# Kernel optimization log

Measured on AMD Instinct MI355X. Metric: run time of the kernel, lower is better.

The kernel has to match this reference:

```python
import jax, jax.numpy as jnp
import numpy as np

B, S, H = 8, 4096, 1024
E, K = 64, 2
CAP_FACTOR = 1.25
TEMP = 1.0
LBW = 0.01


def setup_inputs() -> dict:
    key = jax.random.key(0)
    k1, k2, k3 = jax.random.split(key, 3)
    x = jax.random.normal(k1, (B, S, H), dtype=jnp.float32)
    gate_w = jax.random.normal(k2, (E, H), dtype=jnp.float32) * 0.02
    expert_w = jax.random.normal(k3, (E, H, H), dtype=jnp.float32) * 0.02
    return {"x": x, "gate_w": gate_w, "expert_w": expert_w}


def _moe_forward(x, gate_w, expert_w):
    b, s, h = x.shape
    xf = x.reshape(-1, h)                      # [N, H]
    N = xf.shape[0]
    capacity = int(N * K / E * CAP_FACTOR)

    # --- gating ---
    logits = xf @ gate_w.T                     # [N, E]
    vals, idx = jax.lax.top_k(logits / TEMP, K)  # [N, K]
    probs = jax.nn.softmax(vals, axis=-1)      # [N, K]

    # --- dispatch: first-come-first-served position within each expert ---
    ef = idx.reshape(-1)                       # [N*K], token-major order (matches torch loop)
    onehot = jax.nn.one_hot(ef, E, dtype=jnp.int32)            # [N*K, E]
    pos = jnp.take_along_axis(jnp.cumsum(onehot, axis=0), ef[:, None], axis=1)[:, 0] - 1
    valid = pos < capacity
    slot = jnp.where(valid, ef * capacity + pos, E * capacity)  # out-of-range -> dropped

    # token_map[e, c] = token_idx * K + k  (or -1 if empty)
    token_map = jnp.full((E * capacity,), -1, dtype=jnp.int32)
    token_map = token_map.at[slot].set(jnp.arange(N * K, dtype=jnp.int32), mode="drop")

    tok = jnp.clip(token_map // K, 0, N - 1)
    filled = token_map >= 0
    expert_inputs = jnp.where(filled[:, None], xf[tok], 0.0)    # [E*cap, H]
    expert_inputs = expert_inputs.reshape(E, capacity, h)

    # --- grouped expert GEMM (no bias; zero rows stay zero) ---
    expert_outputs = jnp.einsum("ech,edh->ecd", expert_inputs, expert_w)  # [E, cap, H]

    # --- combine: weighted scatter-add back to tokens ---
    eo_flat = expert_outputs.reshape(E * capacity, h)
    wk = token_map % K
    weight = jnp.where(filled, probs[tok, jnp.clip(wk, 0, K - 1)], 0.0)
    out_idx = jnp.where(filled, tok, N)        # invalid -> dropped
    output = jnp.zeros((N, h), dtype=xf.dtype).at[out_idx].add(
        weight[:, None] * eo_flat, mode="drop")

    # --- aux load-balancing loss ---
    gate_probs = jax.nn.softmax(logits, axis=-1)
    usage = jnp.bincount(ef, length=E).astype(jnp.float32) / (N * K + 1e-9)
    importance = gate_probs.mean(axis=0)
    aux = jnp.sum(usage * importance) * E
    aux = jnp.minimum(aux * LBW, 1.0)

    return output.reshape(b, s, h), aux


def reference(x, gate_w, expert_w):
    return _moe_forward(x, gate_w, expert_w)
```

## Files before the change

kernel.cpp:

```cpp
#include <hip/hip_runtime.h>
#include <hip/hip_bf16.h>

#define NTOK 32768
#define NE 64
#define HD 1024
#define CAP 1280
#define NKF (NTOK*2)
#define NSLOT (NE*CAP)
#define NTILE 128

typedef __attribute__((ext_vector_type(8))) short bf16x8;
typedef __attribute__((ext_vector_type(4))) short bf16x4;
typedef __attribute__((ext_vector_type(4))) float f32x4;
typedef __attribute__((ext_vector_type(4))) unsigned short u16x4;

__device__ __forceinline__ short f2bf(float f) {
  union { __hip_bfloat16 b; short s; } u;
  u.b = __float2bfloat16(f);
  return u.s;
}
__device__ __forceinline__ float bf2f(unsigned short h) {
  return __uint_as_float(((unsigned)h) << 16);
}

__global__ __launch_bounds__(256) void gating_kernel(const float* __restrict__ x,
                                                     const float* __restrict__ gw,
                                                     float* __restrict__ logits,
                                                     __hip_bfloat16* __restrict__ xb) {
  __shared__ float Xs[64][132];
  __shared__ float Gs[64][132];
  const int tid = threadIdx.x;
  const int tok0 = blockIdx.x * 64;
  const int th = tid >> 4;
  const int te = tid & 15;
  float acc[4][4];
#pragma unroll
  for (int i = 0; i < 4; ++i)
#pragma unroll
    for (int j = 0; j < 4; ++j) acc[i][j] = 0.f;

  for (int k0 = 0; k0 < HD; k0 += 128) {
#pragma unroll
    for (int r = 0; r < 8; ++r) {
      int idx = r * 256 + tid;
      int row = idx >> 5;
      int c = (idx & 31) * 4;
      float4 xv4 = *(const float4*)&x[(size_t)(tok0 + row) * HD + k0 + c];
      *(float4*)&Xs[row][c] = xv4;
      bf16x4 o;
      o[0] = f2bf(xv4.x); o[1] = f2bf(xv4.y); o[2] = f2bf(xv4.z); o[3] = f2bf(xv4.w);
      *(bf16x4*)&xb[(size_t)(tok0 + row) * HD + k0 + c] = o;
      *(float4*)&Gs[row][c] = *(const float4*)&gw[(size_t)row * HD + k0 + c];
    }
    __syncthreads();
#pragma unroll 4
    for (int kk = 0; kk < 32; ++kk) {
      float4 xv[4], gv[4];
#pragma unroll
      for (int i = 0; i < 4; ++i) xv[i] = *(float4*)&Xs[th + i * 16][kk * 4];
#pragma unroll
      for (int j = 0; j < 4; ++j) gv[j] = *(float4*)&Gs[te + j * 16][kk * 4];
#pragma unroll
      for (int i = 0; i < 4; ++i)
#pragma unroll
        for (int j = 0; j < 4; ++j) {
          acc[i][j] = fmaf(xv[i].x, gv[j].x, acc[i][j]);
          acc[i][j] = fmaf(xv[i].y, gv[j].y, acc[i][j]);
          acc[i][j] = fmaf(xv[i].z, gv[j].z, acc[i][j]);
          acc[i][j] = fmaf(xv[i].w, gv[j].w, acc[i][j]);
        }
    }
    __syncthreads();
  }
#pragma unroll
  for (int i = 0; i < 4; ++i)
#pragma unroll
    for (int j = 0; j < 4; ++j)
      logits[(size_t)(tok0 + th + i * 16) * NE + te + j * 16] = acc[i][j];
}

__global__ __launch_bounds__(256) void topk_hist_kernel(const float* __restrict__ logits,
                                                        int2* __restrict__ e01,
                                                        float2* __restrict__ p01,
                                                        float* __restrict__ imp_part,
                                                        int* __restrict__ rank_buf,
                                                        int* __restrict__ hist) {
  __shared__ int wh[4][64];
  const int tid = threadIdx.x;
  const int w = tid >> 6, lane = tid & 63;
  const int t = blockIdx.x * 256 + tid;
  float l[64];
  const float4* lp = (const float4*)(logits + (size_t)t * NE);
#pragma unroll
  for (int i = 0; i < 16; ++i) {
    float4 v = lp[i];
    l[4 * i] = v.x; l[4 * i + 1] = v.y; l[4 * i + 2] = v.z; l[4 * i + 3] = v.w;
  }
  float v1 = -1e30f; int i1 = 0;
#pragma unroll
  for (int j = 0; j < 64; ++j) if (l[j] > v1) { v1 = l[j]; i1 = j; }
  float v2 = -1e30f; int i2 = 0;
#pragma unroll
  for (int j = 0; j < 64; ++j) if (j != i1 && l[j] > v2) { v2 = l[j]; i2 = j; }
  float ex = __expf(v2 - v1);
  float inv2 = 1.f / (1.f + ex);
  e01[t] = make_int2(i1, i2);
  p01[t] = make_float2(inv2, ex * inv2);

  float s = 0.f;
#pragma unroll
  for (int j = 0; j < 64; ++j) s += __expf(l[j] - v1);
  float invs = 1.f / s;
  const int wid = t >> 6;
#pragma unroll
  for (int e = 0; e < 64; ++e) {
    float p = __expf(l[e] - v1) * invs;
#pragma unroll
    for (int off = 32; off; off >>= 1) p += __shfl_xor(p, off);
    if (lane == 0) imp_part[(size_t)wid * 64 + e] = p;
  }

  int r0 = 0, r1 = 0, cnt = 0;
#pragma unroll
  for (int j = 0; j < 64; ++j) {
    int a = __shfl(i1, j);
    int b = __shfl(i2, j);
    int ja = (j < lane);
    r0 += ja & (a == i1);
    r0 += ja & (b == i1);
    r1 += ja & (a == i2);
    r1 += ja & (b == i2);
    cnt += (a == lane) + (b == lane);
  }
  wh[w][lane] = cnt;
  __syncthreads();
#pragma unroll
  for (int ww = 0; ww < 4; ++ww)
    if (ww < w) { r0 += wh[ww][i1]; r1 += wh[ww][i2]; }
  rank_buf[2 * t] = r0;
  rank_buf[2 * t + 1] = r1;
  if (tid < 64)
    hist[blockIdx.x * 64 + tid] = wh[0][tid] + wh[1][tid] + wh[2][tid] + wh[3][tid];
}

__global__ __launch_bounds__(64) void scan_kernel(const int* __restrict__ hist,
                                                  int* __restrict__ tile_off,
                                                  int* __restrict__ counts) {
  const int e = threadIdx.x;
  int run = 0;
  for (int t = 0; t < NTILE; ++t) {
    int h = hist[t * 64 + e];
    tile_off[t * 64 + e] = run;
    run += h;
  }
  counts[e] = run;
}

__global__ __launch_bounds__(256) void place_kernel(const int2* __restrict__ e01,
                                                    const int* __restrict__ rank_buf,
                                                    const int* __restrict__ tile_off,
                                                    int* __restrict__ slot_of,
                                                    int* __restrict__ slot_token) {
  const int tid = threadIdx.x;
  const int i = blockIdx.x * 256 + tid;
  int2 ee = e01[i >> 1];
  const int e = (i & 1) ? ee.y : ee.x;
  const int pos = tile_off[(i >> 9) * 64 + e] + rank_buf[i];
  const int slot = (pos < CAP) ? (e * CAP + pos) : -1;
  slot_of[i] = slot;
  if (slot >= 0) slot_token[slot] = i;
}

__global__ __launch_bounds__(256) void convw_kernel(const float* __restrict__ w,
                                                    __hip_bfloat16* __restrict__ wb) {
  size_t i = ((size_t)blockIdx.x * 256 + threadIdx.x) * 8;
  const size_t stride = (size_t)2048 * 256 * 8;
#pragma unroll 2
  for (int it = 0; it < 16; ++it, i += stride) {
    float4 a = *(const float4*)(w + i);
    float4 b = *(const float4*)(w + i + 4);
    bf16x8 o;
    o[0] = f2bf(a.x); o[1] = f2bf(a.y); o[2] = f2bf(a.z); o[3] = f2bf(a.w);
    o[4] = f2bf(b.x); o[5] = f2bf(b.y); o[6] = f2bf(b.z); o[7] = f2bf(b.w);
    *(bf16x8*)(wb + i) = o;
  }
}

#define ASYNC16(g, l) __builtin_amdgcn_global_load_lds( \
    (const __attribute__((address_space(1))) void*)(g), \
    (__attribute__((address_space(3))) void*)(l), 16, 0, 0)

#define STAGE_A(buf, ks, kcol) do {                                             \
    const int _d = ((buf) * 16384 + (ks) * 8192 + wuni) * 2;                    \
    ASYNC16(arow0 + (kcol) + (ks) * 32 + sw8, (char*)lds + _d);                 \
    ASYNC16(arow1 + (kcol) + (ks) * 32 + sw8, (char*)lds + _d + 8192);          \
  } while (0)

#define STAGE_B(buf, ks, kcol) do {                                             \
    const __hip_bfloat16* _g = B + (size_t)srow * HD + (kcol) + (ks) * 32 + sw8; \
    const int _d = (32768 + (buf) * 16384 + (ks) * 8192 + wuni) * 2;            \
    ASYNC16(_g, (char*)lds + _d);                                               \
    ASYNC16(_g + (size_t)128 * HD, (char*)lds + _d + 8192);                     \
  } while (0)

#define LDA(dst, buf, ks, mi) \
  dst = *(const bf16x8*)(lds + (buf) * 16384 + (ks) * 8192 + (wm * 128 + (mi) * 16 + fr) * 32 + rsw)
#define LDB(dst, buf, ks, ni) \
  dst = *(const bf16x8*)(lds + 32768 + (buf) * 16384 + (ks) * 8192 + (wn * 64 + (ni) * 16 + fr) * 32 + rsw)

#define MFMA_HALF(h)                                                            \
  _Pragma("unroll")                                                             \
  for (int mm = 0; mm < 4; ++mm)                                                \
    _Pragma("unroll")                                                           \
    for (int nn = 0; nn < 4; ++nn)                                              \
      acc[(h) * 4 + mm][nn] =                                                   \
          __builtin_amdgcn_mfma_f32_16x16x32_bf16(av[mm], bv[nn], acc[(h) * 4 + mm][nn], 0, 0, 0)

#define BARX() do { asm volatile("" ::: "memory"); __builtin_amdgcn_s_barrier(); asm volatile("" ::: "memory"); } while (0)

__global__ __launch_bounds__(512, 2) void moe_gemm_kernel(const __hip_bfloat16* __restrict__ xb,
                                                          const int* __restrict__ slot_token,
                                                          const __hip_bfloat16* __restrict__ Wb,
                                                          const __hip_bfloat16* __restrict__ zp,
                                                          const int* __restrict__ counts,
                                                          __hip_bfloat16* __restrict__ Eo) {
  __shared__ __hip_bfloat16 lds[65536];

  const int bid = blockIdx.x;
  const int swz = (bid & 7) * 160 + (bid >> 3);
  const int e = swz / 20;
  const int t20 = swz - e * 20;
  const int tm = t20 >> 2, tn = t20 & 3;

  if (tm * 256 >= counts[e]) return;

  const int tid = threadIdx.x;
  const int lane = tid & 63;
  const int w = tid >> 6;
  const int wm = w >> 2, wn = w & 3;

  const __hip_bfloat16* B = Wb + (size_t)e * HD * HD + (size_t)(tn * 256) * HD;

  const int srow = tid >> 2;
  const int sw8 = ((tid & 3) ^ ((tid >> 3) & 3)) * 8;
  const int wuni = w * 512;

  const int slotbase = e * CAP + tm * 256;
  const int i0 = slot_token[slotbase + srow];
  const int i1 = slot_token[slotbase + 128 + srow];
  const __hip_bfloat16* arow0 = (i0 >= 0) ? xb + (size_t)(i0 >> 1) * HD : zp;
  const __hip_bfloat16* arow1 = (i1 >= 0) ? xb + (size_t)(i1 >> 1) * HD : zp;

  const int fr = lane & 15;
  const int fq = lane >> 4;
  const int rsw = (fq ^ ((fr >> 1) & 3)) * 8;

  f32x4 acc[8][4] = {};

  STAGE_A(0, 0, 0);
  STAGE_B(0, 0, 0);
  STAGE_A(0, 1, 0);
  STAGE_B(0, 1, 0);
  asm volatile("s_waitcnt vmcnt(4)" ::: "memory");
  BARX();

#pragma unroll 2
  for (int t = 0; t < 16; ++t) {
    const int cur = t & 1, nxt = cur ^ 1;
    const int kc = (t + 1) * 64;
    const bool hn = (t < 15);
    bf16x8 av[4], bv[4];

    LDB(bv[0], cur, 0, 0); LDB(bv[1], cur, 0, 1); LDB(bv[2], cur, 0, 2); LDB(bv[3], cur, 0, 3);
    LDA(av[0], cur, 0, 0); LDA(av[1], cur, 0, 1); LDA(av[2], cur, 0, 2); LDA(av[3], cur, 0, 3);
    if (hn) STAGE_A(nxt, 0, kc);
    BARX();
    __builtin_amdgcn_s_setprio(1);
    MFMA_HALF(0);
    __builtin_amdgcn_s_setprio(0);
    BARX();

    LDA(av[0], cur, 0, 4); LDA(av[1], cur, 0, 5); LDA(av[2], cur, 0, 6); LDA(av[3], cur, 0, 7);
    if (hn) {
      STAGE_B(nxt, 0, kc);
      asm volatile("s_waitcnt vmcnt(4)" ::: "memory");
    } else {
      asm volatile("s_waitcnt vmcnt(0)" ::: "memory");
    }
    BARX();
    __builtin_amdgcn_s_setprio(1);
    MFMA_HALF(1);
    __builtin_amdgcn_s_setprio(0);
    BARX();

    LDB(bv[0], cur, 1, 0); LDB(bv[1], cur, 1, 1); LDB(bv[2], cur, 1, 2); LDB(bv[3], cur, 1, 3);
    LDA(av[0], cur, 1, 0); LDA(av[1], cur, 1, 1); LDA(av[2], cur, 1, 2); LDA(av[3], cur, 1, 3);
    if (hn) STAGE_A(nxt, 1, kc);
    BARX();
    __builtin_amdgcn_s_setprio(1);
    MFMA_HALF(0);
    __builtin_amdgcn_s_setprio(0);
    BARX();

    LDA(av[0], cur, 1, 4); LDA(av[1], cur, 1, 5); LDA(av[2], cur, 1, 6); LDA(av[3], cur, 1, 7);
    if (hn) {
      STAGE_B(nxt, 1, kc);
      asm volatile("s_waitcnt vmcnt(4)" ::: "memory");
    }
    BARX();
    __builtin_amdgcn_s_setprio(1);
    MFMA_HALF(1);
    __builtin_amdgcn_s_setprio(0);
    BARX();
  }

  __hip_bfloat16* C = Eo + (size_t)e * CAP * HD +
                      (size_t)(tm * 256 + wm * 128) * HD + tn * 256 + wn * 64;
#pragma unroll
  for (int m = 0; m < 8; ++m)
#pragma unroll
    for (int n = 0; n < 4; ++n)
#pragma unroll
      for (int r = 0; r < 4; ++r)
        C[(size_t)(m * 16 + fq * 4 + r) * HD + n * 16 + fr] = __float2bfloat16(acc[m][n][r]);
}

__global__ __launch_bounds__(256) void combine_kernel(const __hip_bfloat16* __restrict__ eo,
                                                      const int* __restrict__ slot_of,
                                                      const float2* __restrict__ p01,
                                                      float* __restrict__ out) {
  const int t = blockIdx.x;
  const int tid = threadIdx.x;
  const float2 p = p01[t];
  const int s0 = slot_of[2 * t], s1 = slot_of[2 * t + 1];
  float a0 = 0.f, a1 = 0.f, a2 = 0.f, a3 = 0.f;
  if (s0 >= 0) {
    u16x4 v = *(const u16x4*)((const unsigned short*)eo + (size_t)s0 * HD + tid * 4);
    a0 += p.x * bf2f(v[0]); a1 += p.x * bf2f(v[1]);
    a2 += p.x * bf2f(v[2]); a3 += p.x * bf2f(v[3]);
  }
  if (s1 >= 0) {
    u16x4 v = *(const u16x4*)((const unsigned short*)eo + (size_t)s1 * HD + tid * 4);
    a0 += p.y * bf2f(v[0]); a1 += p.y * bf2f(v[1]);
    a2 += p.y * bf2f(v[2]); a3 += p.y * bf2f(v[3]);
  }
  float4 res = make_float4(a0, a1, a2, a3);
  *(float4*)(out + (size_t)t * HD + tid * 4) = res;
}

__global__ __launch_bounds__(64) void aux_kernel(const float* __restrict__ imp_part,
                                                 const int* __restrict__ counts,
                                                 float* __restrict__ out) {
  const int e = threadIdx.x;
  float imp = 0.f;
  for (int w = 0; w < 512; ++w) imp += imp_part[(size_t)w * 64 + e];
  imp *= (1.f / (float)NTOK);
  float usage = (float)counts[e] / (float)NKF;
  float v = usage * imp;
#pragma unroll
  for (int off = 32; off; off >>= 1) v += __shfl_xor(v, off);
  if (e == 0) out[(size_t)NTOK * HD] = fminf(v * (float)NE * 0.01f, 1.0f);
}

extern "C" void kernel_launch(void* const* d_in, const int* in_sizes, int n_in,
                              void* d_out, int out_size, void* d_ws, size_t ws_size,
                              hipStream_t stream) {
  const float* x = (const float*)d_in[0];
  const float* gw = (const float*)d_in[1];
  const float* ew = (const float*)d_in[2];
  float* out = (float*)d_out;

  char* p = (char*)d_ws;
  float* logits = (float*)p;            p += (size_t)NTOK * NE * 4;
  int2* e01 = (int2*)p;                 p += (size_t)NTOK * 8;
  float2* p01 = (float2*)p;             p += (size_t)NTOK * 8;
  int* slot_of = (int*)p;               p += (size_t)NKF * 4;
  int* slot_token = (int*)p;            p += (size_t)NSLOT * 4;
  int* counts = (int*)p;                p += 256;
  float* imp_part = (float*)p;          p += (size_t)512 * 64 * 4;
  int* rank_buf = (int*)p;              p += (size_t)NKF * 4;
  int* hist = (int*)p;                  p += (size_t)NTILE * 64 * 4;
  int* tile_off = (int*)p;              p += (size_t)NTILE * 64 * 4;
  __hip_bfloat16* zp = (__hip_bfloat16*)p; p += 4096;
  __hip_bfloat16* xb = (__hip_bfloat16*)p; p += (size_t)NTOK * HD * 2;
  __hip_bfloat16* Wb = (__hip_bfloat16*)p;  p += (size_t)NE * HD * HD * 2;
  __hip_bfloat16* Eo = (__hip_bfloat16*)p;  p += (size_t)NSLOT * HD * 2;

  hipMemsetAsync(slot_token, 0xFF, (size_t)NSLOT * 4, stream);
  hipMemsetAsync(zp, 0, 4096, stream);

  gating_kernel<<<NTOK / 64, 256, 0, stream>>>(x, gw, logits, xb);
  topk_hist_kernel<<<NTOK / 256, 256, 0, stream>>>(logits, e01, p01, imp_part, rank_buf, hist);
  scan_kernel<<<1, 64, 0, stream>>>(hist, tile_off, counts);
  place_kernel<<<NKF / 256, 256, 0, stream>>>(e01, rank_buf, tile_off, slot_of, slot_token);
  convw_kernel<<<2048, 256, 0, stream>>>(ew, Wb);
  moe_gemm_kernel<<<dim3(1280), 512, 0, stream>>>(xb, slot_token, Wb, zp, counts, Eo);
  combine_kernel<<<NTOK, 256, 0, stream>>>(Eo, slot_of, p01, out);
  aux_kernel<<<1, 64, 0, stream>>>(imp_part, counts, out);
}
```

Measured before the change: 445.9 us.

## Fuse fp32-to-bf16 weight conversion into expert GEMM B-tile staging

Removes the separate weight-conversion kernel and its bf16 weight buffer. The GEMM now loads fp32 expert weights into registers, converts them to bf16 and writes them to LDS, instead of copying pre-converted bf16 tiles asynchronously. This saves a full read and write pass over the 256 MB fp32 weight tensor and one launch. In exchange each GEMM block reads twice as many bytes for B, uses more registers, and waits on vmcnt(0) each iteration, which may weaken load/compute overlap. Weight tiles are re-read by every m-tile of an expert, so the extra fp32 traffic repeats across m-tiles.

```diff
diff --git a/kernel.cpp b/kernel.cpp
--- a/kernel.cpp
+++ b/kernel.cpp
@@ -171,21 +171,6 @@
   if (slot >= 0) slot_token[slot] = i;
 }
 
-__global__ __launch_bounds__(256) void convw_kernel(const float* __restrict__ w,
-                                                    __hip_bfloat16* __restrict__ wb) {
-  size_t i = ((size_t)blockIdx.x * 256 + threadIdx.x) * 8;
-  const size_t stride = (size_t)2048 * 256 * 8;
-#pragma unroll 2
-  for (int it = 0; it < 16; ++it, i += stride) {
-    float4 a = *(const float4*)(w + i);
-    float4 b = *(const float4*)(w + i + 4);
-    bf16x8 o;
-    o[0] = f2bf(a.x); o[1] = f2bf(a.y); o[2] = f2bf(a.z); o[3] = f2bf(a.w);
-    o[4] = f2bf(b.x); o[5] = f2bf(b.y); o[6] = f2bf(b.z); o[7] = f2bf(b.w);
-    *(bf16x8*)(wb + i) = o;
-  }
-}
-
 #define ASYNC16(g, l) __builtin_amdgcn_global_load_lds( \
     (const __attribute__((address_space(1))) void*)(g), \
     (__attribute__((address_space(3))) void*)(l), 16, 0, 0)
@@ -196,11 +181,27 @@
     ASYNC16(arow1 + (kcol) + (ks) * 32 + sw8, (char*)lds + _d + 8192);          \
   } while (0)
 
-#define STAGE_B(buf, ks, kcol) do {                                             \
-    const __hip_bfloat16* _g = B + (size_t)srow * HD + (kcol) + (ks) * 32 + sw8; \
-    const int _d = (32768 + (buf) * 16384 + (ks) * 8192 + wuni) * 2;            \
-    ASYNC16(_g, (char*)lds + _d);                                               \
-    ASYNC16(_g + (size_t)128 * HD, (char*)lds + _d + 8192);                     \
+#define BWRITE(buf, ks, p0, p1, p2, p3) do {                                    \
+    bf16x8 o;                                                                   \
+    o[0] = f2bf((p0).x); o[1] = f2bf((p0).y); o[2] = f2bf((p0).z); o[3] = f2bf((p0).w); \
+    o[4] = f2bf((p1).x); o[5] = f2bf((p1).y); o[6] = f2bf((p1).z); o[7] = f2bf((p1).w); \
+    *(bf16x8*)(lds + 32768 + (buf) * 16384 + (ks) * 8192 + srow * 32 + sw8) = o; \
+    bf16x8 o2;                                                                  \
+    o2[0] = f2bf((p2).x); o2[1] = f2bf((p2).y); o2[2] = f2bf((p2).z); o2[3] = f2bf((p2).w); \
+    o2[4] = f2bf((p3).x); o2[5] = f2bf((p3).y); o2[6] = f2bf((p3).z); o2[7] = f2bf((p3).w); \
+    *(bf16x8*)(lds + 32768 + (buf) * 16384 + (ks) * 8192 + (srow + 128) * 32 + sw8) = o2; \
+  } while (0)
+
+#define BLOADS(kcol) do {                                                       \
+    const float* _g = Bf + (kcol);                                              \
+    b00 = *(const float4*)(_g);                                                 \
+    b01 = *(const float4*)(_g + 4);                                             \
+    b02 = *(const float4*)(_g + (size_t)128 * HD);                              \
+    b03 = *(const float4*)(_g + (size_t)128 * HD + 4);                          \
+    b10 = *(const float4*)(_g + 32);                                            \
+    b11 = *(const float4*)(_g + 36);                                            \
+    b12 = *(const float4*)(_g + (size_t)128 * HD + 32);                         \
+    b13 = *(const float4*)(_g + (size_t)128 * HD + 36);                         \
   } while (0)
 
 #define LDA(dst, buf, ks, mi) \
@@ -217,10 +218,12 @@
           __builtin_amdgcn_mfma_f32_16x16x32_bf16(av[mm], bv[nn], acc[(h) * 4 + mm][nn], 0, 0, 0)
 
 #define BARX() do { asm volatile("" ::: "memory"); __builtin_amdgcn_s_barrier(); asm volatile("" ::: "memory"); } while (0)
+#define LGKM0() asm volatile("s_waitcnt lgkmcnt(0)" ::: "memory")
+#define VM0()   asm volatile("s_waitcnt vmcnt(0)" ::: "memory")
 
 __global__ __launch_bounds__(512, 2) void moe_gemm_kernel(const __hip_bfloat16* __restrict__ xb,
                                                           const int* __restrict__ slot_token,
-                                                          const __hip_bfloat16* __restrict__ Wb,
+                                                          const float* __restrict__ ew,
                                                           const __hip_bfloat16* __restrict__ zp,
                                                           const int* __restrict__ counts,
                                                           __hip_bfloat16* __restrict__ Eo) {
@@ -239,8 +242,6 @@
   const int w = tid >> 6;
   const int wm = w >> 2, wn = w & 3;
 
-  const __hip_bfloat16* B = Wb + (size_t)e * HD * HD + (size_t)(tn * 256) * HD;
-
   const int srow = tid >> 2;
   const int sw8 = ((tid & 3) ^ ((tid >> 3) & 3)) * 8;
   const int wuni = w * 512;
@@ -251,17 +252,22 @@
   const __hip_bfloat16* arow0 = (i0 >= 0) ? xb + (size_t)(i0 >> 1) * HD : zp;
   const __hip_bfloat16* arow1 = (i1 >= 0) ? xb + (size_t)(i1 >> 1) * HD : zp;
 
+  const float* Bf = ew + (size_t)e * HD * HD + (size_t)(tn * 256 + srow) * HD + (tid & 3) * 8;
+
   const int fr = lane & 15;
   const int fq = lane >> 4;
   const int rsw = (fq ^ ((fr >> 1) & 3)) * 8;
 
   f32x4 acc[8][4] = {};
-
+  float4 b00, b01, b02, b03, b10, b11, b12, b13;
+
+  BLOADS(0);
   STAGE_A(0, 0, 0);
-  STAGE_B(0, 0, 0);
   STAGE_A(0, 1, 0);
-  STAGE_B(0, 1, 0);
-  asm volatile("s_waitcnt vmcnt(4)" ::: "memory");
+  BWRITE(0, 0, b00, b01, b02, b03);
+  BWRITE(0, 1, b10, b11, b12, b13);
+  VM0();
+  LGKM0();
   BARX();
 
 #pragma unroll 2
@@ -273,7 +279,11 @@
 
     LDB(bv[0], cur, 0, 0); LDB(bv[1], cur, 0, 1); LDB(bv[2], cur, 0, 2); LDB(bv[3], cur, 0, 3);
     LDA(av[0], cur, 0, 0); LDA(av[1], cur, 0, 1); LDA(av[2], cur, 0, 2); LDA(av[3], cur, 0, 3);
-    if (hn) STAGE_A(nxt, 0, kc);
+    if (hn) {
+      BLOADS(kc);
+      STAGE_A(nxt, 0, kc);
+      STAGE_A(nxt, 1, kc);
+    }
     BARX();
     __builtin_amdgcn_s_setprio(1);
     MFMA_HALF(0);
@@ -282,10 +292,8 @@
 
     LDA(av[0], cur, 0, 4); LDA(av[1], cur, 0, 5); LDA(av[2], cur, 0, 6); LDA(av[3], cur, 0, 7);
     if (hn) {
-      STAGE_B(nxt, 0, kc);
-      asm volatile("s_waitcnt vmcnt(4)" ::: "memory");
-    } else {
-      asm volatile("s_waitcnt vmcnt(0)" ::: "memory");
+      BWRITE(nxt, 0, b00, b01, b02, b03);
+      LGKM0();
     }
     BARX();
     __builtin_amdgcn_s_setprio(1);
@@ -295,7 +303,10 @@
 
     LDB(bv[0], cur, 1, 0); LDB(bv[1], cur, 1, 1); LDB(bv[2], cur, 1, 2); LDB(bv[3], cur, 1, 3);
     LDA(av[0], cur, 1, 0); LDA(av[1], cur, 1, 1); LDA(av[2], cur, 1, 2); LDA(av[3], cur, 1, 3);
-    if (hn) STAGE_A(nxt, 1, kc);
+    if (hn) {
+      BWRITE(nxt, 1, b10, b11, b12, b13);
+      LGKM0();
+    }
     BARX();
     __builtin_amdgcn_s_setprio(1);
     MFMA_HALF(0);
@@ -303,10 +314,7 @@
     BARX();
 
     LDA(av[0], cur, 1, 4); LDA(av[1], cur, 1, 5); LDA(av[2], cur, 1, 6); LDA(av[3], cur, 1, 7);
-    if (hn) {
-      STAGE_B(nxt, 1, kc);
-      asm volatile("s_waitcnt vmcnt(4)" ::: "memory");
-    }
+    if (hn) VM0();
     BARX();
     __builtin_amdgcn_s_setprio(1);
     MFMA_HALF(1);
@@ -383,7 +391,6 @@
   int* tile_off = (int*)p;              p += (size_t)NTILE * 64 * 4;
   __hip_bfloat16* zp = (__hip_bfloat16*)p; p += 4096;
   __hip_bfloat16* xb = (__hip_bfloat16*)p; p += (size_t)NTOK * HD * 2;
-  __hip_bfloat16* Wb = (__hip_bfloat16*)p;  p += (size_t)NE * HD * HD * 2;
   __hip_bfloat16* Eo = (__hip_bfloat16*)p;  p += (size_t)NSLOT * HD * 2;
 
   hipMemsetAsync(slot_token, 0xFF, (size_t)NSLOT * 4, stream);
@@ -393,8 +400,7 @@
   topk_hist_kernel<<<NTOK / 256, 256, 0, stream>>>(logits, e01, p01, imp_part, rank_buf, hist);
   scan_kernel<<<1, 64, 0, stream>>>(hist, tile_off, counts);
   place_kernel<<<NKF / 256, 256, 0, stream>>>(e01, rank_buf, tile_off, slot_of, slot_token);
-  convw_kernel<<<2048, 256, 0, stream>>>(ew, Wb);
-  moe_gemm_kernel<<<dim3(1280), 512, 0, stream>>>(xb, slot_token, Wb, zp, counts, Eo);
+  moe_gemm_kernel<<<dim3(1280), 512, 0, stream>>>(xb, slot_token, ew, zp, counts, Eo);
   combine_kernel<<<NTOK, 256, 0, stream>>>(Eo, slot_of, p01, out);
   aux_kernel<<<1, 64, 0, stream>>>(imp_part, counts, out);
 }
```

After: 685.5 us. 1.54x slower.
